# Kernel tuning notes

Measured on AMD Instinct MI355X. Metric: run time of the kernel, lower is better.

The kernel has to match this reference:

```python
import jax, jax.numpy as jnp
import numpy as np

V = 500000
VD = 256
G = 4000
H = 8
GD = 256
HIDDEN = 128


def setup_inputs() -> dict:
    key = jax.random.key(0)
    ks = jax.random.split(key, 6)
    node_embeddings = jax.random.normal(ks[0], (V, VD), dtype=jnp.float32)
    node_to_graph_map = jnp.sort(jax.random.randint(ks[1], (V,), 0, G, dtype=jnp.int32))
    scale = lambda fan_in: 1.0 / np.sqrt(fan_in)
    scoring_w1 = jax.random.normal(ks[2], (VD, HIDDEN), dtype=jnp.float32) * scale(VD)
    scoring_w2 = jax.random.normal(ks[3], (HIDDEN, H), dtype=jnp.float32) * scale(HIDDEN)
    transform_w1 = jax.random.normal(ks[4], (VD, HIDDEN), dtype=jnp.float32) * scale(VD)
    transform_w2 = jax.random.normal(ks[5], (HIDDEN, GD), dtype=jnp.float32) * scale(HIDDEN)
    return {
        "node_embeddings": node_embeddings,
        "node_to_graph_map": node_to_graph_map,
        "num_graphs": G,
        "scoring_w1": scoring_w1,
        "scoring_w2": scoring_w2,
        "transform_w1": transform_w1,
        "transform_w2": transform_w2,
    }


def _segment_softmax(logits, segment_ids, num_segments):
    # logits: [V, H]; softmax over nodes within each graph, per head.
    seg_max = jax.ops.segment_max(logits, segment_ids, num_segments=num_segments)
    seg_max = jnp.where(jnp.isfinite(seg_max), seg_max, 0.0)
    exp = jnp.exp(logits - seg_max[segment_ids])
    denom = jax.ops.segment_sum(exp, segment_ids, num_segments=num_segments)
    return exp / denom[segment_ids]


def reference(node_embeddings, node_to_graph_map, num_graphs,
              scoring_w1, scoring_w2, transform_w1, transform_w2):
    # Scoring MLP (hidden ReLU, linear out, no biases): [V, H]
    scores = jax.nn.relu(node_embeddings @ scoring_w1) @ scoring_w2
    # Per-graph softmax weights, per head: [V, H]
    weights = _segment_softmax(scores, node_to_graph_map, num_graphs)
    # Transformation MLP, then the call() applies the activation to the MLP output.
    node_reprs = jax.nn.relu(jax.nn.relu(node_embeddings @ transform_w1) @ transform_w2)  # [V, GD]
    node_reprs = node_reprs.reshape(-1, H, GD // H)  # [V, H, GD/H]
    weighted = (weights[:, :, None] * node_reprs).reshape(-1, GD)  # [V, GD]
    graph_reprs = jax.ops.segment_sum(weighted, node_to_graph_map, num_segments=num_graphs)
    return graph_reprs
```

## Files before the change

kernel.cpp:

```cpp
#include <hip/hip_runtime.h>
#include <hip/hip_fp16.h>

#define VD 256
#define HID 128
#define GD 256
#define NH 8
#define NGRAPH 4000
#define RT 64

typedef _Float16 f16;
typedef f16 f16x4 __attribute__((ext_vector_type(4)));
typedef f16 f16x8 __attribute__((ext_vector_type(8)));
typedef float f32x4 __attribute__((ext_vector_type(4)));

__device__ __forceinline__ f16x8 load_a_frag(const float* p) {
  float4 p0 = *(const float4*)(p);
  float4 p1 = *(const float4*)(p + 4);
  f16x8 v;
  v[0] = (f16)p0.x; v[1] = (f16)p0.y; v[2] = (f16)p0.z; v[3] = (f16)p0.w;
  v[4] = (f16)p1.x; v[5] = (f16)p1.y; v[6] = (f16)p1.z; v[7] = (f16)p1.w;
  return v;
}

__device__ __forceinline__ void pack_b_dev(const float* __restrict__ src,
                                           f16* __restrict__ dst,
                                           int K, int Nsrc, int Ndst, int t) {
  int NB = Ndst / 16, KB = K / 32;
  int total = KB * NB * 64;
  if (t >= total) return;
  int lane = t & 63;
  int frag = t >> 6;
  int nb = frag % NB, kb = frag / NB;
  int col = nb * 16 + (lane & 15);
  int krow = kb * 32 + (lane >> 4) * 8;
  f16x8 o;
  #pragma unroll
  for (int i = 0; i < 8; ++i) {
    float v = (col < Nsrc) ? src[(size_t)(krow + i) * Nsrc + col] : 0.0f;
    o[i] = (f16)v;
  }
  *(f16x8*)(dst + (size_t)t * 8) = o;
}

__global__ __launch_bounds__(256) void k_prep(
    const float* __restrict__ w1s, const float* __restrict__ w1t,
    const float* __restrict__ w2t, const float* __restrict__ w2s,
    const int* __restrict__ map,
    f16* __restrict__ W1sp, f16* __restrict__ W1tp,
    f16* __restrict__ W2tp, f16* __restrict__ W2sp,
    int* __restrict__ gs, int V, int G) {
  int b = blockIdx.x;
  int tid = threadIdx.x;
  if (b < 16) {
    pack_b_dev(w1s, W1sp, VD, HID, HID, b * 256 + tid);
  } else if (b < 32) {
    pack_b_dev(w1t, W1tp, VD, HID, HID, (b - 16) * 256 + tid);
  } else if (b < 48) {
    pack_b_dev(w2t, W2tp, HID, GD, GD, (b - 32) * 256 + tid);
  } else if (b == 48) {
    pack_b_dev(w2s, W2sp, HID, NH, 16, tid);
  } else {
    int g = (b - 49) * 256 + tid;
    if (g > G) return;
    int lo = 0, hi = V;
    while (lo < hi) {
      int mid = (lo + hi) >> 1;
      if (map[mid] < g) lo = mid + 1; else hi = mid;
    }
    gs[g] = lo;
  }
}

__global__ __launch_bounds__(512, 4) void k_stage1(
    const float* __restrict__ E, int V, int ntiles,
    const f16* __restrict__ W1sp, const f16* __restrict__ W2sp,
    const f16* __restrict__ W1tp,
    float* __restrict__ scores, f16* __restrict__ ht) {
  __shared__ __attribute__((aligned(16))) f16 lE[RT][VD + 8];
  __shared__ __attribute__((aligned(16))) f16 lH[RT][HID + 8];
  __shared__ __attribute__((aligned(16))) f16 lT[RT][HID + 8];
  const int tid = threadIdx.x;
  const int wave = tid >> 6;
  const int lane = tid & 63;
  const int hi = lane >> 4;
  const int lo = lane & 15;
  const int srow = tid >> 6;
  const int scol = (tid & 63) * 4;

  f16x8 Bs[8], Bt[8];
  #pragma unroll
  for (int kb = 0; kb < 8; ++kb) {
    Bs[kb] = *(const f16x8*)(W1sp + ((size_t)(kb * 8 + wave) * 64 + lane) * 8);
    Bt[kb] = *(const f16x8*)(W1tp + ((size_t)(kb * 8 + wave) * 64 + lane) * 8);
  }

  int t = blockIdx.x;
  if (t >= ntiles) return;
  const int stride = gridDim.x;

  float4 pf[8];
  {
    const int r0 = t * RT;
    #pragma unroll
    for (int p = 0; p < 8; ++p) {
      int grow = r0 + p * 8 + srow;
      pf[p] = (grow < V) ? *(const float4*)(E + (size_t)grow * VD + scol)
                         : make_float4(0.f, 0.f, 0.f, 0.f);
    }
  }

  while (t < ntiles) {
    const int r0 = t * RT;
    #pragma unroll
    for (int p = 0; p < 8; ++p) {
      f16x4 h;
      h[0] = (f16)pf[p].x; h[1] = (f16)pf[p].y;
      h[2] = (f16)pf[p].z; h[3] = (f16)pf[p].w;
      *(f16x4*)&lE[p * 8 + srow][scol] = h;
    }
    const int tn = t + stride;
    if (tn < ntiles) {
      const int rn = tn * RT;
      #pragma unroll
      for (int p = 0; p < 8; ++p) {
        int grow = rn + p * 8 + srow;
        pf[p] = (grow < V) ? *(const float4*)(E + (size_t)grow * VD + scol)
                           : make_float4(0.f, 0.f, 0.f, 0.f);
      }
    }
    __syncthreads();

    #pragma unroll
    for (int m = 0; m < 4; ++m) {
      f32x4 as = {0.f, 0.f, 0.f, 0.f};
      f32x4 at = {0.f, 0.f, 0.f, 0.f};
      #pragma unroll
      for (int kb = 0; kb < 8; ++kb) {
        f16x8 a = *(const f16x8*)&lE[m * 16 + lo][kb * 32 + hi * 8];
        as = __builtin_amdgcn_mfma_f32_16x16x32_f16(a, Bs[kb], as, 0, 0, 0);
        at = __builtin_amdgcn_mfma_f32_16x16x32_f16(a, Bt[kb], at, 0, 0, 0);
      }
      #pragma unroll
      for (int r = 0; r < 4; ++r) {
        lH[m * 16 + hi * 4 + r][wave * 16 + lo] = (f16)fmaxf(as[r], 0.f);
        if (ht != nullptr)
          lT[m * 16 + hi * 4 + r][wave * 16 + lo] = (f16)fmaxf(at[r], 0.f);
      }
    }
    __syncthreads();

    if (wave < 4) {
      f16x8 a2[4];
      #pragma unroll
      for (int kb = 0; kb < 4; ++kb)
        a2[kb] = *(const f16x8*)&lH[wave * 16 + lo][kb * 32 + hi * 8];
      f32x4 acc = {0.f, 0.f, 0.f, 0.f};
      #pragma unroll
      for (int kb = 0; kb < 4; ++kb) {
        f16x8 b = *(const f16x8*)(W2sp + ((size_t)kb * 64 + lane) * 8);
        acc = __builtin_amdgcn_mfma_f32_16x16x32_f16(a2[kb], b, acc, 0, 0, 0);
      }
      if (lo < NH) {
        #pragma unroll
        for (int r = 0; r < 4; ++r) {
          int row = r0 + wave * 16 + hi * 4 + r;
          if (row < V) scores[(size_t)row * NH + lo] = acc[r];
        }
      }
    }

    if (ht != nullptr) {
      #pragma unroll
      for (int p = 0; p < 2; ++p) {
        int c = p * 512 + tid;
        int row = c >> 4;
        int col = (c & 15) * 8;
        int grow = r0 + row;
        if (grow < V)
          *(f16x8*)(ht + (size_t)grow * HID + col) = *(const f16x8*)&lT[row][col];
      }
    }
    t = tn;
  }
}

__global__ __launch_bounds__(256, 4) void k_graph(
    const f16* __restrict__ ht, const float* __restrict__ scores,
    const f16* __restrict__ W2tp, const int* __restrict__ gs,
    float* __restrict__ out, int V) {
  __shared__ float red[4][NH];
  const int g = blockIdx.x;
  const int tid = threadIdx.x;
  const int wave = tid >> 6;
  const int lane = tid & 63;
  const int hi = lane >> 4;
  const int lo = lane & 15;
  const int s = gs[g], e = gs[g + 1];

  f16x8 b[4][4];
  #pragma unroll
  for (int j = 0; j < 4; ++j)
    #pragma unroll
    for (int kb = 0; kb < 4; ++kb)
      b[j][kb] = *(const f16x8*)(
          W2tp + ((size_t)(kb * 16 + wave * 4 + j) * 64 + lane) * 8);

  float mx[NH];
  #pragma unroll
  for (int h = 0; h < NH; ++h) mx[h] = -1e30f;
  for (int i = s + tid; i < e; i += 256) {
    float4 s0 = *(const float4*)(scores + (size_t)i * NH);
    float4 s1 = *(const float4*)(scores + (size_t)i * NH + 4);
    mx[0] = fmaxf(mx[0], s0.x); mx[1] = fmaxf(mx[1], s0.y);
    mx[2] = fmaxf(mx[2], s0.z); mx[3] = fmaxf(mx[3], s0.w);
    mx[4] = fmaxf(mx[4], s1.x); mx[5] = fmaxf(mx[5], s1.y);
    mx[6] = fmaxf(mx[6], s1.z); mx[7] = fmaxf(mx[7], s1.w);
  }
  #pragma unroll
  for (int off = 32; off >= 1; off >>= 1)
    #pragma unroll
    for (int h = 0; h < NH; ++h) mx[h] = fmaxf(mx[h], __shfl_xor(mx[h], off));
  if (lane == 0) {
    #pragma unroll
    for (int h = 0; h < NH; ++h) red[wave][h] = mx[h];
  }
  __syncthreads();
  #pragma unroll
  for (int h = 0; h < NH; ++h)
    mx[h] = fmaxf(fmaxf(red[0][h], red[1][h]), fmaxf(red[2][h], red[3][h]));
  __syncthreads();

  float sm[NH];
  #pragma unroll
  for (int h = 0; h < NH; ++h) sm[h] = 0.f;
  for (int i = s + tid; i < e; i += 256) {
    float4 s0 = *(const float4*)(scores + (size_t)i * NH);
    float4 s1 = *(const float4*)(scores + (size_t)i * NH + 4);
    sm[0] += __expf(s0.x - mx[0]); sm[1] += __expf(s0.y - mx[1]);
    sm[2] += __expf(s0.z - mx[2]); sm[3] += __expf(s0.w - mx[3]);
    sm[4] += __expf(s1.x - mx[4]); sm[5] += __expf(s1.y - mx[5]);
    sm[6] += __expf(s1.z - mx[6]); sm[7] += __expf(s1.w - mx[7]);
  }
  #pragma unroll
  for (int off = 32; off >= 1; off >>= 1)
    #pragma unroll
    for (int h = 0; h < NH; ++h) sm[h] += __shfl_xor(sm[h], off);
  if (lane == 0) {
    #pragma unroll
    for (int h = 0; h < NH; ++h) red[wave][h] = sm[h];
  }
  __syncthreads();

  const int h0 = wave * 2, h1 = wave * 2 + 1;
  const float m0 = mx[h0], m1 = mx[h1];
  const float ri0 = 1.f / (red[0][h0] + red[1][h0] + red[2][h0] + red[3][h0]);
  const float ri1 = 1.f / (red[0][h1] + red[1][h1] + red[2][h1] + red[3][h1]);

  float vsum[4] = {0.f, 0.f, 0.f, 0.f};

  for (int cb = s; cb < e; cb += 16) {
    f16x8 a[4];
    int arow = cb + lo;
    int ar = arow < V ? arow : V - 1;
    #pragma unroll
    for (int kb = 0; kb < 4; ++kb)
      a[kb] = *(const f16x8*)(ht + (size_t)ar * HID + kb * 32 + hi * 8);

    int wr = cb + hi * 4;
    float wv[2][4];
    #pragma unroll
    for (int r = 0; r < 4; ++r) {
      int row = wr + r;
      bool in = row < e;
      float sc0 = in ? scores[(size_t)row * NH + h0] : 0.f;
      float sc1 = in ? scores[(size_t)row * NH + h1] : 0.f;
      wv[0][r] = in ? __expf(sc0 - m0) * ri0 : 0.f;
      wv[1][r] = in ? __expf(sc1 - m1) * ri1 : 0.f;
    }
    #pragma unroll
    for (int j = 0; j < 4; ++j) {
      f32x4 acc = {0.f, 0.f, 0.f, 0.f};
      #pragma unroll
      for (int kb = 0; kb < 4; ++kb)
        acc = __builtin_amdgcn_mfma_f32_16x16x32_f16(a[kb], b[j][kb], acc, 0, 0, 0);
      const float* wvp = wv[j >> 1];
      float v = 0.f;
      #pragma unroll
      for (int r = 0; r < 4; ++r) v += fmaxf(acc[r], 0.f) * wvp[r];
      vsum[j] += v;
    }
  }

  #pragma unroll
  for (int j = 0; j < 4; ++j) {
    float v = vsum[j];
    v += __shfl_xor(v, 16);
    v += __shfl_xor(v, 32);
    if (lane < 16) out[(size_t)g * GD + (wave * 4 + j) * 16 + lo] = v;
  }
}

__global__ __launch_bounds__(64) void k_stats(
    float* __restrict__ scores, const int* __restrict__ gs) {
  int g = blockIdx.x;
  int lane = threadIdx.x;
  int s = gs[g], e = gs[g + 1];
  if (e <= s) return;
  float mx[NH];
  #pragma unroll
  for (int h = 0; h < NH; ++h) mx[h] = -1e30f;
  for (int i = s + lane; i < e; i += 64) {
    float4 s0 = *(const float4*)(scores + (size_t)i * NH);
    float4 s1 = *(const float4*)(scores + (size_t)i * NH + 4);
    mx[0] = fmaxf(mx[0], s0.x); mx[1] = fmaxf(mx[1], s0.y);
    mx[2] = fmaxf(mx[2], s0.z); mx[3] = fmaxf(mx[3], s0.w);
    mx[4] = fmaxf(mx[4], s1.x); mx[5] = fmaxf(mx[5], s1.y);
    mx[6] = fmaxf(mx[6], s1.z); mx[7] = fmaxf(mx[7], s1.w);
  }
  #pragma unroll
  for (int off = 32; off >= 1; off >>= 1)
    #pragma unroll
    for (int h = 0; h < NH; ++h) mx[h] = fmaxf(mx[h], __shfl_xor(mx[h], off));
  float sm[NH];
  #pragma unroll
  for (int h = 0; h < NH; ++h) sm[h] = 0.f;
  for (int i = s + lane; i < e; i += 64) {
    float4 s0 = *(const float4*)(scores + (size_t)i * NH);
    float4 s1 = *(const float4*)(scores + (size_t)i * NH + 4);
    sm[0] += __expf(s0.x - mx[0]); sm[1] += __expf(s0.y - mx[1]);
    sm[2] += __expf(s0.z - mx[2]); sm[3] += __expf(s0.w - mx[3]);
    sm[4] += __expf(s1.x - mx[4]); sm[5] += __expf(s1.y - mx[5]);
    sm[6] += __expf(s1.z - mx[6]); sm[7] += __expf(s1.w - mx[7]);
  }
  #pragma unroll
  for (int off = 32; off >= 1; off >>= 1)
    #pragma unroll
    for (int h = 0; h < NH; ++h) sm[h] += __shfl_xor(sm[h], off);
  float rinv[NH];
  #pragma unroll
  for (int h = 0; h < NH; ++h) rinv[h] = 1.f / sm[h];
  for (int i = s + lane; i < e; i += 64) {
    float4 s0 = *(const float4*)(scores + (size_t)i * NH);
    float4 s1 = *(const float4*)(scores + (size_t)i * NH + 4);
    s0.x = __expf(s0.x - mx[0]) * rinv[0]; s0.y = __expf(s0.y - mx[1]) * rinv[1];
    s0.z = __expf(s0.z - mx[2]) * rinv[2]; s0.w = __expf(s0.w - mx[3]) * rinv[3];
    s1.x = __expf(s1.x - mx[4]) * rinv[4]; s1.y = __expf(s1.y - mx[5]) * rinv[5];
    s1.z = __expf(s1.z - mx[6]) * rinv[6]; s1.w = __expf(s1.w - mx[7]) * rinv[7];
    *(float4*)(scores + (size_t)i * NH) = s0;
    *(float4*)(scores + (size_t)i * NH + 4) = s1;
  }
}

__global__ __launch_bounds__(256, 2) void k_transform2(
    const float* __restrict__ E, int V,
    const f16* __restrict__ W1tp, const f16* __restrict__ W2tp,
    const float* __restrict__ w, const int* __restrict__ gs,
    float* __restrict__ out) {
  __shared__ f16 hl[16][HID + 8];
  const int g = blockIdx.x;
  const int wave = threadIdx.x >> 6;
  const int lane = threadIdx.x & 63;
  const int hi = lane >> 4;
  const int lo = lane & 15;
  const int s = gs[g], e = gs[g + 1];

  f16x8 b[4][4];
  #pragma unroll
  for (int j = 0; j < 4; ++j)
    #pragma unroll
    for (int kb = 0; kb < 4; ++kb)
      b[j][kb] = *(const f16x8*)(
          W2tp + ((size_t)(kb * 16 + wave * 4 + j) * 64 + lane) * 8);

  float vsum[4] = {0.f, 0.f, 0.f, 0.f};

  for (int cb = s; cb < e; cb += 16) {
    int arow = cb + lo;
    int ar = arow < V ? arow : V - 1;
    f16x8 a[8];
    const float* ep = E + (size_t)ar * VD + hi * 8;
    #pragma unroll
    for (int kb = 0; kb < 8; ++kb) a[kb] = load_a_frag(ep + kb * 32);

    __syncthreads();
    #pragma unroll
    for (int nn = 0; nn < 2; ++nn) {
      int n = wave * 2 + nn;
      f32x4 acc = {0.f, 0.f, 0.f, 0.f};
      #pragma unroll
      for (int kb = 0; kb < 8; ++kb) {
        f16x8 bb = *(const f16x8*)(W1tp + ((size_t)(kb * 8 + n) * 64 + lane) * 8);
        acc = __builtin_amdgcn_mfma_f32_16x16x32_f16(a[kb], bb, acc, 0, 0, 0);
      }
      #pragma unroll
      for (int r = 0; r < 4; ++r)
        hl[hi * 4 + r][n * 16 + lo] = (f16)fmaxf(acc[r], 0.f);
    }
    __syncthreads();

    int wr = cb + hi * 4;
    float wv[2][4];
    #pragma unroll
    for (int hh = 0; hh < 2; ++hh) {
      int head = wave * 2 + hh;
      #pragma unroll
      for (int r = 0; r < 4; ++r) {
        int row = wr + r;
        wv[hh][r] = (row < e) ? w[(size_t)row * NH + head] : 0.f;
      }
    }
    f16x8 a2[4];
    #pragma unroll
    for (int kb = 0; kb < 4; ++kb)
      a2[kb] = *(const f16x8*)&hl[lo][kb * 32 + hi * 8];
    #pragma unroll
    for (int j = 0; j < 4; ++j) {
      f32x4 acc = {0.f, 0.f, 0.f, 0.f};
      #pragma unroll
      for (int kb = 0; kb < 4; ++kb)
        acc = __builtin_amdgcn_mfma_f32_16x16x32_f16(a2[kb], b[j][kb], acc, 0, 0, 0);
      const float* wvp = wv[j >> 1];
      float v = 0.f;
      #pragma unroll
      for (int r = 0; r < 4; ++r) v += fmaxf(acc[r], 0.f) * wvp[r];
      vsum[j] += v;
    }
  }

  #pragma unroll
  for (int j = 0; j < 4; ++j) {
    float v = vsum[j];
    v += __shfl_xor(v, 16);
    v += __shfl_xor(v, 32);
    if (lane < 16) out[(size_t)g * GD + (wave * 4 + j) * 16 + lo] = v;
  }
}

extern "C" void kernel_launch(void* const* d_in, const int* in_sizes, int n_in,
                              void* d_out, int out_size, void* d_ws, size_t ws_size,
                              hipStream_t stream) {
  const float* E   = (const float*)d_in[0];
  const int*   map = (const int*)d_in[1];
  const float* w1s = (const float*)d_in[3];
  const float* w2s = (const float*)d_in[4];
  const float* w1t = (const float*)d_in[5];
  const float* w2t = (const float*)d_in[6];
  const int V = in_sizes[0] / VD;
  const int G = NGRAPH;

  char* ws = (char*)d_ws;
  size_t off = 0;
  float* scores = (float*)(ws + off); off += (size_t)V * NH * 4;
  int* gs = (int*)(ws + off); off += (size_t)(G + 1) * 4;
  off = (off + 255) & ~(size_t)255;
  f16* W1sp = (f16*)(ws + off); off += (size_t)VD * HID * 2;
  f16* W1tp = (f16*)(ws + off); off += (size_t)VD * HID * 2;
  f16* W2tp = (f16*)(ws + off); off += (size_t)HID * GD * 2;
  f16* W2sp = (f16*)(ws + off); off += (size_t)HID * 16 * 2;
  off = (off + 255) & ~(size_t)255;
  f16* ht = (f16*)(ws + off);
  const size_t need_fused = off + (size_t)V * HID * 2;
  const bool fused = ws_size >= need_fused;

  k_prep<<<65, 256, 0, stream>>>(w1s, w1t, w2t, w2s, map,
                                 W1sp, W1tp, W2tp, W2sp, gs, V, G);

  const int ntiles = (V + RT - 1) / RT;
  const int grid1 = (ntiles + 3) / 4;
  k_stage1<<<grid1, 512, 0, stream>>>(
      E, V, ntiles, W1sp, W2sp, W1tp, scores, fused ? ht : nullptr);

  if (fused) {
    k_graph<<<G, 256, 0, stream>>>(ht, scores, W2tp, gs, (float*)d_out, V);
  } else {
    k_stats<<<G, 64, 0, stream>>>(scores, gs);
    k_transform2<<<G, 256, 0, stream>>>(E, V, W1tp, W2tp, scores, gs,
                                        (float*)d_out);
  }
}
```

Baseline: 288.7 us.

## Replace per-graph phase-2 kernel with node-chunk kernel using atomic segment reduction

The per-graph k_graph kernel is replaced by k_stats (in-place softmax normalization) plus a new k_phase2v kernel. It tiles over fixed 64-node chunks and scatters per-graph partial sums into a zeroed output with atomicAdd. This targets load imbalance and under-utilization from one block per graph with variable segment sizes, at the cost of an extra memset, an extra kernel launch and float atomics, which make the summation order nondeterministic. Stage1 also splits its A-fragment loads into two batches of four, and moves the ht store to the otherwise idle upper waves.

```diff
diff --git a/kernel.cpp b/kernel.cpp
--- a/kernel.cpp
+++ b/kernel.cpp
@@ -134,17 +134,27 @@
     for (int m = 0; m < 4; ++m) {
       f32x4 as = {0.f, 0.f, 0.f, 0.f};
       f32x4 at = {0.f, 0.f, 0.f, 0.f};
-      #pragma unroll
-      for (int kb = 0; kb < 8; ++kb) {
-        f16x8 a = *(const f16x8*)&lE[m * 16 + lo][kb * 32 + hi * 8];
-        as = __builtin_amdgcn_mfma_f32_16x16x32_f16(a, Bs[kb], as, 0, 0, 0);
-        at = __builtin_amdgcn_mfma_f32_16x16x32_f16(a, Bt[kb], at, 0, 0, 0);
+      f16x8 a4[4];
+      #pragma unroll
+      for (int kb = 0; kb < 4; ++kb)
+        a4[kb] = *(const f16x8*)&lE[m * 16 + lo][kb * 32 + hi * 8];
+      #pragma unroll
+      for (int kb = 0; kb < 4; ++kb) {
+        as = __builtin_amdgcn_mfma_f32_16x16x32_f16(a4[kb], Bs[kb], as, 0, 0, 0);
+        at = __builtin_amdgcn_mfma_f32_16x16x32_f16(a4[kb], Bt[kb], at, 0, 0, 0);
+      }
+      #pragma unroll
+      for (int kb = 0; kb < 4; ++kb)
+        a4[kb] = *(const f16x8*)&lE[m * 16 + lo][(kb + 4) * 32 + hi * 8];
+      #pragma unroll
+      for (int kb = 0; kb < 4; ++kb) {
+        as = __builtin_amdgcn_mfma_f32_16x16x32_f16(a4[kb], Bs[kb + 4], as, 0, 0, 0);
+        at = __builtin_amdgcn_mfma_f32_16x16x32_f16(a4[kb], Bt[kb + 4], at, 0, 0, 0);
       }
       #pragma unroll
       for (int r = 0; r < 4; ++r) {
         lH[m * 16 + hi * 4 + r][wave * 16 + lo] = (f16)fmaxf(as[r], 0.f);
-        if (ht != nullptr)
-          lT[m * 16 + hi * 4 + r][wave * 16 + lo] = (f16)fmaxf(at[r], 0.f);
+        lT[m * 16 + hi * 4 + r][wave * 16 + lo] = (f16)fmaxf(at[r], 0.f);
       }
     }
     __syncthreads();
@@ -167,12 +177,11 @@
           if (row < V) scores[(size_t)row * NH + lo] = acc[r];
         }
       }
-    }
-
-    if (ht != nullptr) {
-      #pragma unroll
-      for (int p = 0; p < 2; ++p) {
-        int c = p * 512 + tid;
+    } else if (ht != nullptr) {
+      const int base = tid - 256;
+      #pragma unroll
+      for (int p = 0; p < 4; ++p) {
+        int c = p * 256 + base;
         int row = c >> 4;
         int col = (c & 15) * 8;
         int grow = r0 + row;
@@ -181,122 +190,6 @@
       }
     }
     t = tn;
-  }
-}
-
-__global__ __launch_bounds__(256, 4) void k_graph(
-    const f16* __restrict__ ht, const float* __restrict__ scores,
-    const f16* __restrict__ W2tp, const int* __restrict__ gs,
-    float* __restrict__ out, int V) {
-  __shared__ float red[4][NH];
-  const int g = blockIdx.x;
-  const int tid = threadIdx.x;
-  const int wave = tid >> 6;
-  const int lane = tid & 63;
-  const int hi = lane >> 4;
-  const int lo = lane & 15;
-  const int s = gs[g], e = gs[g + 1];
-
-  f16x8 b[4][4];
-  #pragma unroll
-  for (int j = 0; j < 4; ++j)
-    #pragma unroll
-    for (int kb = 0; kb < 4; ++kb)
-      b[j][kb] = *(const f16x8*)(
-          W2tp + ((size_t)(kb * 16 + wave * 4 + j) * 64 + lane) * 8);
-
-  float mx[NH];
-  #pragma unroll
-  for (int h = 0; h < NH; ++h) mx[h] = -1e30f;
-  for (int i = s + tid; i < e; i += 256) {
-    float4 s0 = *(const float4*)(scores + (size_t)i * NH);
-    float4 s1 = *(const float4*)(scores + (size_t)i * NH + 4);
-    mx[0] = fmaxf(mx[0], s0.x); mx[1] = fmaxf(mx[1], s0.y);
-    mx[2] = fmaxf(mx[2], s0.z); mx[3] = fmaxf(mx[3], s0.w);
-    mx[4] = fmaxf(mx[4], s1.x); mx[5] = fmaxf(mx[5], s1.y);
-    mx[6] = fmaxf(mx[6], s1.z); mx[7] = fmaxf(mx[7], s1.w);
-  }
-  #pragma unroll
-  for (int off = 32; off >= 1; off >>= 1)
-    #pragma unroll
-    for (int h = 0; h < NH; ++h) mx[h] = fmaxf(mx[h], __shfl_xor(mx[h], off));
-  if (lane == 0) {
-    #pragma unroll
-    for (int h = 0; h < NH; ++h) red[wave][h] = mx[h];
-  }
-  __syncthreads();
-  #pragma unroll
-  for (int h = 0; h < NH; ++h)
-    mx[h] = fmaxf(fmaxf(red[0][h], red[1][h]), fmaxf(red[2][h], red[3][h]));
-  __syncthreads();
-
-  float sm[NH];
-  #pragma unroll
-  for (int h = 0; h < NH; ++h) sm[h] = 0.f;
-  for (int i = s + tid; i < e; i += 256) {
-    float4 s0 = *(const float4*)(scores + (size_t)i * NH);
-    float4 s1 = *(const float4*)(scores + (size_t)i * NH + 4);
-    sm[0] += __expf(s0.x - mx[0]); sm[1] += __expf(s0.y - mx[1]);
-    sm[2] += __expf(s0.z - mx[2]); sm[3] += __expf(s0.w - mx[3]);
-    sm[4] += __expf(s1.x - mx[4]); sm[5] += __expf(s1.y - mx[5]);
-    sm[6] += __expf(s1.z - mx[6]); sm[7] += __expf(s1.w - mx[7]);
-  }
-  #pragma unroll
-  for (int off = 32; off >= 1; off >>= 1)
-    #pragma unroll
-    for (int h = 0; h < NH; ++h) sm[h] += __shfl_xor(sm[h], off);
-  if (lane == 0) {
-    #pragma unroll
-    for (int h = 0; h < NH; ++h) red[wave][h] = sm[h];
-  }
-  __syncthreads();
-
-  const int h0 = wave * 2, h1 = wave * 2 + 1;
-  const float m0 = mx[h0], m1 = mx[h1];
-  const float ri0 = 1.f / (red[0][h0] + red[1][h0] + red[2][h0] + red[3][h0]);
-  const float ri1 = 1.f / (red[0][h1] + red[1][h1] + red[2][h1] + red[3][h1]);
-
-  float vsum[4] = {0.f, 0.f, 0.f, 0.f};
-
-  for (int cb = s; cb < e; cb += 16) {
-    f16x8 a[4];
-    int arow = cb + lo;
-    int ar = arow < V ? arow : V - 1;
-    #pragma unroll
-    for (int kb = 0; kb < 4; ++kb)
-      a[kb] = *(const f16x8*)(ht + (size_t)ar * HID + kb * 32 + hi * 8);
-
-    int wr = cb + hi * 4;
-    float wv[2][4];
-    #pragma unroll
-    for (int r = 0; r < 4; ++r) {
-      int row = wr + r;
-      bool in = row < e;
-      float sc0 = in ? scores[(size_t)row * NH + h0] : 0.f;
-      float sc1 = in ? scores[(size_t)row * NH + h1] : 0.f;
-      wv[0][r] = in ? __expf(sc0 - m0) * ri0 : 0.f;
-      wv[1][r] = in ? __expf(sc1 - m1) * ri1 : 0.f;
-    }
-    #pragma unroll
-    for (int j = 0; j < 4; ++j) {
-      f32x4 acc = {0.f, 0.f, 0.f, 0.f};
-      #pragma unroll
-      for (int kb = 0; kb < 4; ++kb)
-        acc = __builtin_amdgcn_mfma_f32_16x16x32_f16(a[kb], b[j][kb], acc, 0, 0, 0);
-      const float* wvp = wv[j >> 1];
-      float v = 0.f;
-      #pragma unroll
-      for (int r = 0; r < 4; ++r) v += fmaxf(acc[r], 0.f) * wvp[r];
-      vsum[j] += v;
-    }
-  }
-
-  #pragma unroll
-  for (int j = 0; j < 4; ++j) {
-    float v = vsum[j];
-    v += __shfl_xor(v, 16);
-    v += __shfl_xor(v, 32);
-    if (lane < 16) out[(size_t)g * GD + (wave * 4 + j) * 16 + lo] = v;
   }
 }
 
@@ -348,6 +241,74 @@
     s1.z = __expf(s1.z - mx[6]) * rinv[6]; s1.w = __expf(s1.w - mx[7]) * rinv[7];
     *(float4*)(scores + (size_t)i * NH) = s0;
     *(float4*)(scores + (size_t)i * NH + 4) = s1;
+  }
+}
+
+__global__ __launch_bounds__(256, 4) void k_phase2v(
+    const f16* __restrict__ ht, const float* __restrict__ w,
+    const f16* __restrict__ W2tp, const int* __restrict__ map,
+    float* __restrict__ out, int V) {
+  const int wave = threadIdx.x >> 6;
+  const int lane = threadIdx.x & 63;
+  const int hi = lane >> 4;
+  const int lo = lane & 15;
+  const int rb0 = blockIdx.x * 64;
+  const int h0 = wave * 2;
+
+  f16x8 b[4][4];
+  #pragma unroll
+  for (int nb = 0; nb < 4; ++nb)
+    #pragma unroll
+    for (int kb = 0; kb < 4; ++kb)
+      b[nb][kb] = *(const f16x8*)(
+          W2tp + ((size_t)(kb * 16 + wave * 4 + nb) * 64 + lane) * 8);
+
+  #pragma unroll
+  for (int m = 0; m < 4; ++m) {
+    const int rb = rb0 + m * 16;
+    if (rb >= V) break;
+    f16x8 a[4];
+    {
+      int arow = rb + lo;
+      int ar = arow < V ? arow : V - 1;
+      #pragma unroll
+      for (int kb = 0; kb < 4; ++kb)
+        a[kb] = *(const f16x8*)(ht + (size_t)ar * HID + kb * 32 + hi * 8);
+    }
+    float wv0[4], wv1[4];
+    int gr[4];
+    #pragma unroll
+    for (int r = 0; r < 4; ++r) {
+      int row = rb + hi * 4 + r;
+      bool in = row < V;
+      int rc = in ? row : V - 1;
+      gr[r] = map[rc];
+      wv0[r] = in ? w[(size_t)rc * NH + h0] : 0.f;
+      wv1[r] = in ? w[(size_t)rc * NH + h0 + 1] : 0.f;
+    }
+    const int gfirst = __shfl(gr[0], 0);
+    const int glast = __shfl(gr[3], 48);
+
+    #pragma unroll
+    for (int nb = 0; nb < 4; ++nb) {
+      f32x4 acc = {0.f, 0.f, 0.f, 0.f};
+      #pragma unroll
+      for (int kb = 0; kb < 4; ++kb)
+        acc = __builtin_amdgcn_mfma_f32_16x16x32_f16(a[kb], b[nb][kb], acc, 0, 0, 0);
+      const float* wvp = (nb < 2) ? wv0 : wv1;
+      float val[4];
+      #pragma unroll
+      for (int r = 0; r < 4; ++r) val[r] = fmaxf(acc[r], 0.f) * wvp[r];
+      const int col = wave * 64 + nb * 16 + lo;
+      for (int g = gfirst; g <= glast; ++g) {
+        float vg = 0.f;
+        #pragma unroll
+        for (int r = 0; r < 4; ++r) vg += (gr[r] == g) ? val[r] : 0.f;
+        vg += __shfl_xor(vg, 16);
+        vg += __shfl_xor(vg, 32);
+        if (lane < 16) atomicAdd(&out[(size_t)g * GD + col], vg);
+      }
+    }
   }
 }
 
@@ -470,10 +431,14 @@
   k_stage1<<<grid1, 512, 0, stream>>>(
       E, V, ntiles, W1sp, W2sp, W1tp, scores, fused ? ht : nullptr);
 
+  k_stats<<<G, 64, 0, stream>>>(scores, gs);
+
   if (fused) {
-    k_graph<<<G, 256, 0, stream>>>(ht, scores, W2tp, gs, (float*)d_out, V);
+    hipMemsetAsync(d_out, 0, (size_t)out_size * sizeof(float), stream);
+    const int nchunks = (V + 63) / 64;
+    k_phase2v<<<nchunks, 256, 0, stream>>>(ht, scores, W2tp, map,
+                                           (float*)d_out, V);
   } else {
-    k_stats<<<G, 64, 0, stream>>>(scores, gs);
     k_transform2<<<G, 256, 0, stream>>>(E, V, W1tp, W2tp, scores, gs,
                                         (float*)d_out);
   }
```

Measured after the change: 507.9 us. 75.9% more time.
